# Kernel tuning notes

Measured on AMD Instinct MI355X. Metric: run time of the kernel, lower is better.

The kernel has to match this reference:

```python
import jax, jax.numpy as jnp
import numpy as np

BS, S, WIDTH, MODES = 2, 512, 64, 16
P = S * (S - 1) // 2
IU, JU = np.triu_indices(S, 1)  # upper-triangle (i<j) index constants
COLL_COEF = 0.9  # training=True path


def spectral_conv(x, w):
    # x: (bs, c_in, n), w: (c_in, c_out, modes, 2)
    n = x.shape[-1]
    xf = jnp.fft.rfft(x, axis=2, norm='ortho')  # (bs, c_in, n//2+1) complex
    wm = w[..., 0] + 1j * w[..., 1]
    out_m = jnp.einsum('bix,iox->box', xf[:, :, :MODES], wm)
    pad = jnp.zeros((x.shape[0], w.shape[1], n // 2 + 1 - MODES), dtype=out_m.dtype)
    return jnp.fft.irfft(jnp.concatenate([out_m, pad], axis=2), n=n, axis=2, norm='ortho')


def dsmc(x, a, rvec):
    # x, a: (bs, c, n); rvec: (bs, c, P) unit vectors along c.  dt=1, v = a*dt.
    bs, c, n = x.shape
    v = a
    x_r = jnp.linalg.norm(x[:, :, :, None] - x[:, :, None, :], axis=1)  # (bs, n, n)
    v_r = jnp.linalg.norm(v[:, :, :, None] - v[:, :, None, :], axis=1)
    v_cm = (v[:, :, :, None] + v[:, :, None, :]) * 0.5  # (bs, c, n, n)
    x_cm = (x[:, :, :, None] + x[:, :, None, :]) * 0.5
    u_x = jnp.exp(-x_r)
    v_r_max = jnp.max(v_r, axis=(1, 2), keepdims=True)  # (bs,1,1)
    mask = v_r / v_r_max * u_x
    cm = mask > (1.0 - COLL_COEF)  # collision mask (bs, n, n)
    # antisymmetric projection of v_r upper triangle onto random unit vectors
    proj = v_r[:, IU, JU][:, None, :] * rvec  # (bs, c, P)
    vrl = (jnp.zeros((bs, c, n, n), x.dtype)
           .at[:, :, IU, JU].set(proj)
           .at[:, :, JU, IU].set(-proj))
    delta_v = v_cm + vrl - v[:, :, :, None]
    cmf = cm.astype(x.dtype)
    v_new = v + jnp.sum(delta_v * cmf[:, None], axis=2)  # sum over partners i
    cmf = cmf + jnp.eye(n, dtype=x.dtype)[None]  # add self
    x_new = jnp.sum(x_cm * cmf[:, None], axis=2) / jnp.sum(cmf, axis=2)[:, None, :]
    x_new = x_new + v_new  # x = x + v*dt
    return x_new, v_new


def setup_inputs() -> dict:
    key = jax.random.key(0)
    ks = jax.random.split(key, 12)
    x = jax.random.normal(ks[0], (BS, S, 2), jnp.float32)
    v = jax.random.normal(ks[1], (BS, WIDTH, S), jnp.float32)
    vecs = jax.random.normal(ks[2], (4, BS, WIDTH, P), jnp.float32)
    vecs = vecs / jnp.linalg.norm(vecs, axis=2, keepdims=True)  # unit vectors over chnl
    fc0_w = jax.random.normal(ks[3], (2, WIDTH), jnp.float32) * 0.5
    fc0_b = jax.random.normal(ks[4], (WIDTH,), jnp.float32) * 0.1
    scale = 1.0 / (WIDTH * WIDTH)
    spec_w = jax.random.uniform(ks[5], (4, WIDTH, WIDTH, MODES, 2), jnp.float32) * scale
    conv_w = jax.random.normal(ks[6], (4, WIDTH, WIDTH), jnp.float32) * (WIDTH ** -0.5)
    conv_b = jax.random.normal(ks[7], (4, WIDTH), jnp.float32) * 0.05
    fc1_w = jax.random.normal(ks[8], (WIDTH, 128), jnp.float32) * (WIDTH ** -0.5)
    fc1_b = jnp.zeros((128,), jnp.float32)
    fc2_w = jax.random.normal(ks[9], (128, 1), jnp.float32) * (128 ** -0.5)
    fc2_b = jnp.zeros((1,), jnp.float32)
    return {"x": x, "v": v, "vecs": vecs, "fc0_w": fc0_w, "fc0_b": fc0_b,
            "spec_w": spec_w, "conv_w": conv_w, "conv_b": conv_b,
            "fc1_w": fc1_w, "fc1_b": fc1_b, "fc2_w": fc2_w, "fc2_b": fc2_b}


def reference(x, v, vecs, fc0_w, fc0_b, spec_w, conv_w, conv_b, fc1_w, fc1_b, fc2_w, fc2_b):
    # NOTE: v is overwritten by a*dt inside KINET_DSMC2 in the original; kept for signature fidelity.
    h = x @ fc0_w + fc0_b          # (bs, s, width)
    h = jnp.transpose(h, (0, 2, 1))  # (bs, width, s)
    for i in range(4):
        a = spectral_conv(h, spec_w[i])
        p = jnp.einsum('oi,bin->bon', conv_w[i], h) + conv_b[i][None, :, None]
        h, vv = dsmc(p, a, vecs[i])
        if i < 3:
            h = jax.nn.relu(h)
    h = jnp.transpose(h, (0, 2, 1))  # (bs, s, width)
    h = jax.nn.relu(h @ fc1_w + fc1_b)
    return h @ fc2_w + fc2_b  # (bs, s, 1)
```

## Files before the change

### kernel.cpp

```cpp
#include <hip/hip_runtime.h>
#include <math.h>

#define S 512
#define W 64
#define MODES 16
#define PAIRS 130816
#define INV_SQRT_N 0.04419417382415922f
#define TWO_PI_OVER_N 0.012271846303085130f

__global__ __launch_bounds__(256) void k_fft(const float* __restrict__ h,
                                             const float* __restrict__ x,
                                             const float* __restrict__ fc0w,
                                             const float* __restrict__ fc0b,
                                             float* __restrict__ Xf, int first) {
    int b = blockIdx.x >> 6, ch = blockIdx.x & 63;
    int tid = threadIdx.x;
    float v0, v1;
    if (first) {
        float w0 = fc0w[ch], w1 = fc0w[64 + ch], bb = fc0b[ch];
        const float* xb = x + (size_t)b * S * 2;
        v0 = xb[2 * tid] * w0 + xb[2 * tid + 1] * w1 + bb;
        v1 = xb[2 * (tid + 256)] * w0 + xb[2 * (tid + 256) + 1] * w1 + bb;
    } else {
        const float* hp = h + (b * W + ch) * S;
        v0 = hp[tid]; v1 = hp[tid + 256];
    }
    float re[MODES], im[MODES];
#pragma unroll
    for (int m = 0; m < MODES; ++m) {
        float sn, cs;
        sincosf(TWO_PI_OVER_N * (float)(m * tid), &sn, &cs);
        float a = (m & 1) ? (v0 - v1) : (v0 + v1);
        re[m] = a * cs;
        im[m] = -a * sn;
    }
    __shared__ float part[4][32];
    int lane = tid & 63, wv = tid >> 6;
#pragma unroll
    for (int m = 0; m < MODES; ++m) {
        float r = re[m], ii = im[m];
        for (int off = 32; off; off >>= 1) {
            r += __shfl_down(r, off);
            ii += __shfl_down(ii, off);
        }
        if (lane == 0) { part[wv][2 * m] = r; part[wv][2 * m + 1] = ii; }
    }
    __syncthreads();
    if (tid < 32) {
        float s = part[0][tid] + part[1][tid] + part[2][tid] + part[3][tid];
        Xf[(b * W + ch) * 32 + tid] = s * INV_SQRT_N;
    }
}

__global__ __launch_bounds__(256) void k_mix(const float* __restrict__ Xf,
                                             const float* __restrict__ specw,
                                             float* __restrict__ Y, int l) {
    int b = blockIdx.x >> 6, o = blockIdx.x & 63;
    int tid = threadIdx.x, m = tid & 15, ip = tid >> 4;
    __shared__ float Xs[2048];
    for (int idx = tid; idx < 2048; idx += 256) Xs[idx] = Xf[b * 2048 + idx];
    __syncthreads();
    float ar = 0.f, ai = 0.f;
#pragma unroll
    for (int q = 0; q < 4; ++q) {
        int i = ip * 4 + q;
        const float* wp = specw + (size_t)(((l * W + i) * W + o) * MODES + m) * 2;
        float wr = wp[0], wi = wp[1];
        float xr = Xs[i * 32 + 2 * m], xi = Xs[i * 32 + 2 * m + 1];
        ar += xr * wr - xi * wi;
        ai += xr * wi + xi * wr;
    }
    __shared__ float redr[16][17], redi[16][17];
    redr[ip][m] = ar; redi[ip][m] = ai;
    __syncthreads();
    if (tid < 16) {
        float sr = 0.f, si = 0.f;
        for (int p = 0; p < 16; ++p) { sr += redr[p][tid]; si += redi[p][tid]; }
        Y[(b * W + o) * 32 + 2 * tid] = sr;
        Y[(b * W + o) * 32 + 2 * tid + 1] = si;
    }
}

__global__ __launch_bounds__(256) void k_ac(const float* __restrict__ Y,
                                            const float* __restrict__ h,
                                            const float* __restrict__ x,
                                            const float* __restrict__ fc0w,
                                            const float* __restrict__ fc0b,
                                            const float* __restrict__ convw,
                                            const float* __restrict__ convb,
                                            float* __restrict__ aT,
                                            float* __restrict__ pT,
                                            unsigned* __restrict__ vmax,
                                            int l, int first) {
    int blk = blockIdx.x;
    int b = blk >> 7, t0 = (blk & 127) * 4;
    int tid = threadIdx.x;
    int o = tid & 63, tg = tid >> 6;
    if (blk == 0 && tid < 2) vmax[tid] = 0u;
    __shared__ float hs[64 * 5];
    {
        int r = tid >> 2, t = tid & 3;
        if (first) {
            const float* xb = x + ((size_t)b * S + t0 + t) * 2;
            hs[r * 5 + t] = xb[0] * fc0w[r] + xb[1] * fc0w[64 + r] + fc0b[r];
        } else {
            hs[r * 5 + t] = h[(b * W + r) * S + t0 + t];
        }
    }
    float yr[MODES], yi[MODES];
    const float4* yp = (const float4*)(Y + b * 2048 + o * 32);
#pragma unroll
    for (int q = 0; q < 8; ++q) {
        float4 y4 = yp[q];
        yr[2 * q] = y4.x; yi[2 * q] = y4.y;
        yr[2 * q + 1] = y4.z; yi[2 * q + 1] = y4.w;
    }
    int t = t0 + tg;
    float acc = yr[0];
#pragma unroll
    for (int m = 1; m < MODES; ++m) {
        float sn, cs;
        sincosf(TWO_PI_OVER_N * (float)(m * t), &sn, &cs);
        acc += 2.0f * (yr[m] * cs - yi[m] * sn);
    }
    aT[((size_t)b * S + t) * W + o] = acc * INV_SQRT_N;
    __syncthreads();
    float pacc = convb[l * W + o];
    const float4* wp = (const float4*)(convw + l * 4096 + o * 64);
#pragma unroll
    for (int i4 = 0; i4 < 16; ++i4) {
        float4 w4 = wp[i4];
        pacc = fmaf(w4.x, hs[(4 * i4 + 0) * 5 + tg], pacc);
        pacc = fmaf(w4.y, hs[(4 * i4 + 1) * 5 + tg], pacc);
        pacc = fmaf(w4.z, hs[(4 * i4 + 2) * 5 + tg], pacc);
        pacc = fmaf(w4.w, hs[(4 * i4 + 3) * 5 + tg], pacc);
    }
    pT[((size_t)b * S + t) * W + o] = pacc;
}

__global__ __launch_bounds__(256) void k_pair(const float* __restrict__ pT,
                                              const float* __restrict__ aT,
                                              float* __restrict__ vr,
                                              float* __restrict__ uxm,
                                              unsigned* __restrict__ vmax) {
    int blk = blockIdx.x;
    int b = blk >> 8;
    int rest = blk & 255;
    int i0 = (rest & 15) * 32, j0 = (rest >> 4) * 32;
    int tid = threadIdx.x;
    int tx = tid & 15, ty = tid >> 4;
    __shared__ float Pi[64 * 33], Pj[64 * 33], Vi[64 * 33], Vj[64 * 33];
    for (int idx = tid; idx < 2048; idx += 256) {
        int k = idx >> 6, c = idx & 63;
        Pi[c * 33 + k] = pT[(b * S + i0 + k) * W + c];
        Pj[c * 33 + k] = pT[(b * S + j0 + k) * W + c];
        Vi[c * 33 + k] = aT[(b * S + i0 + k) * W + c];
        Vj[c * 33 + k] = aT[(b * S + j0 + k) * W + c];
    }
    __syncthreads();
    float ax[2][2] = {{0.f, 0.f}, {0.f, 0.f}};
    float av[2][2] = {{0.f, 0.f}, {0.f, 0.f}};
    for (int c = 0; c < W; ++c) {
        float pi0 = Pi[c * 33 + 2 * tx], pi1 = Pi[c * 33 + 2 * tx + 1];
        float pj0 = Pj[c * 33 + 2 * ty], pj1 = Pj[c * 33 + 2 * ty + 1];
        float vi0 = Vi[c * 33 + 2 * tx], vi1 = Vi[c * 33 + 2 * tx + 1];
        float vj0 = Vj[c * 33 + 2 * ty], vj1 = Vj[c * 33 + 2 * ty + 1];
        float d;
        d = pi0 - pj0; ax[0][0] = fmaf(d, d, ax[0][0]);
        d = pi1 - pj0; ax[1][0] = fmaf(d, d, ax[1][0]);
        d = pi0 - pj1; ax[0][1] = fmaf(d, d, ax[0][1]);
        d = pi1 - pj1; ax[1][1] = fmaf(d, d, ax[1][1]);
        d = vi0 - vj0; av[0][0] = fmaf(d, d, av[0][0]);
        d = vi1 - vj0; av[1][0] = fmaf(d, d, av[1][0]);
        d = vi0 - vj1; av[0][1] = fmaf(d, d, av[0][1]);
        d = vi1 - vj1; av[1][1] = fmaf(d, d, av[1][1]);
    }
    float mx = 0.f;
#pragma unroll
    for (int jj = 0; jj < 2; ++jj) {
#pragma unroll
        for (int ii = 0; ii < 2; ++ii) {
            int i = i0 + 2 * tx + ii, j = j0 + 2 * ty + jj;
            float xr = sqrtf(ax[ii][jj]);
            float vv = sqrtf(av[ii][jj]);
            vr[((size_t)b * S + j) * S + i] = vv;
            uxm[((size_t)b * S + j) * S + i] = expf(-xr);
            mx = fmaxf(mx, vv);
        }
    }
    __shared__ float mxs[4];
    for (int off = 32; off; off >>= 1) mx = fmaxf(mx, __shfl_xor(mx, off));
    if ((tid & 63) == 0) mxs[tid >> 6] = mx;
    __syncthreads();
    if (tid == 0) {
        float m = fmaxf(fmaxf(mxs[0], mxs[1]), fmaxf(mxs[2], mxs[3]));
        atomicMax(&vmax[b], __float_as_uint(m));
    }
}

__global__ __launch_bounds__(256) void k_mpf(const float* __restrict__ vr,
                                             const float* __restrict__ uxm,
                                             const unsigned* __restrict__ vmaxu,
                                             const float* __restrict__ aT,
                                             const float* __restrict__ pT,
                                             const float* __restrict__ vecs,
                                             float* __restrict__ h_std,
                                             const float* __restrict__ fc1w,
                                             const float* __restrict__ fc1b,
                                             const float* __restrict__ fc2w,
                                             const float* __restrict__ fc2b,
                                             float* __restrict__ out,
                                             int l, int do_relu, int do_head) {
    int b = blockIdx.x >> 9, q = blockIdx.x & 511;
    int tid = threadIdx.x, lane = tid & 63, wv = tid >> 6;
    __shared__ float wrow[S];
    __shared__ float SV[4][64], SX[4][64], TP[4][64];
    __shared__ float hrow[64];
    __shared__ int cnt4[4];
    const float* vrp = vr + ((size_t)b * S + q) * S;
    const float* uxp = uxm + ((size_t)b * S + q) * S;
    float vmax = __uint_as_float(vmaxu[b]);
    int mycnt = 0;
    for (int i = tid; i < S; i += 256) {
        float v = vrp[i], u = uxp[i];
        bool act = (v / vmax) * u > 0.1f;
        wrow[i] = act ? v : 0.f;
        mycnt += act ? 1 : 0;
    }
    for (int o = 32; o; o >>= 1) mycnt += __shfl_down(mycnt, o);
    if (lane == 0) cnt4[wv] = mycnt;
    __syncthreads();
    float A = (float)(cnt4[0] + cnt4[1] + cnt4[2] + cnt4[3]);
    float svp = 0.f, sxp = 0.f, tp = 0.f;
    const float* aTb = aT + (size_t)b * S * W;
    const float* pTb = pT + (size_t)b * S * W;
    const float* Rb = vecs + (size_t)((l * 2 + b) * W + lane) * PAIRS;
    int triq = q * 511 - ((q * (q - 1)) >> 1);
    for (int k = 0; k < 128; ++k) {
        int p = wv * 128 + k;
        float w = wrow[p];
        if (w != 0.f) {
            svp += aTb[p * W + lane];
            sxp += pTb[p * W + lane];
            int idx; float sgn;
            if (p < q) { idx = p * 511 - ((p * (p - 1)) >> 1) + (q - p - 1); sgn = 1.f; }
            else       { idx = triq + (p - q - 1); sgn = -1.f; }
            tp = fmaf(sgn * w, Rb[idx], tp);
        }
    }
    SV[wv][lane] = svp; SX[wv][lane] = sxp; TP[wv][lane] = tp;
    __syncthreads();
    if (wv == 0) {
        float sv = SV[0][lane] + SV[1][lane] + SV[2][lane] + SV[3][lane];
        float sx = SX[0][lane] + SX[1][lane] + SX[2][lane] + SX[3][lane];
        float T  = TP[0][lane] + TP[1][lane] + TP[2][lane] + TP[3][lane];
        float vj = aTb[q * W + lane], xj = pTb[q * W + lane];
        float vnew = vj + 0.5f * (A * vj - sv) + T;
        float accx = 0.5f * (A * xj + sx);
        float xnew = (xj + accx) / (A + 1.0f) + vnew;
        if (do_relu) xnew = fmaxf(xnew, 0.0f);
        if (!do_head) h_std[((size_t)b * W + lane) * S + q] = xnew;
        else hrow[lane] = xnew;
    }
    if (do_head) {
        __syncthreads();
        if (wv == 0) {
            float a0 = fc1b[lane], a1 = fc1b[lane + 64];
            for (int cc = 0; cc < W; ++cc) {
                float hv = hrow[cc];
                a0 = fmaf(hv, fc1w[cc * 128 + lane], a0);
                a1 = fmaf(hv, fc1w[cc * 128 + lane + 64], a1);
            }
            a0 = fmaxf(a0, 0.f); a1 = fmaxf(a1, 0.f);
            float p = a0 * fc2w[lane] + a1 * fc2w[lane + 64];
            for (int off = 32; off; off >>= 1) p += __shfl_down(p, off);
            if (lane == 0) out[b * S + q] = p + fc2b[0];
        }
    }
}

extern "C" void kernel_launch(void* const* d_in, const int* in_sizes, int n_in,
                              void* d_out, int out_size, void* d_ws, size_t ws_size,
                              hipStream_t stream) {
    const float* x = (const float*)d_in[0];
    const float* vecs = (const float*)d_in[2];
    const float* fc0w = (const float*)d_in[3];
    const float* fc0b = (const float*)d_in[4];
    const float* specw = (const float*)d_in[5];
    const float* convw = (const float*)d_in[6];
    const float* convb = (const float*)d_in[7];
    const float* fc1w = (const float*)d_in[8];
    const float* fc1b = (const float*)d_in[9];
    const float* fc2w = (const float*)d_in[10];
    const float* fc2b = (const float*)d_in[11];
    float* out = (float*)d_out;

    char* ws = (char*)d_ws;
    unsigned* vmax = (unsigned*)ws;
    float* h_std = (float*)(ws + 256);
    float* aT = h_std + 65536;
    float* pT = aT + 65536;
    float* Xf = pT + 65536;
    float* Yb = Xf + 4096;
    float* vrbuf = Yb + 4096;
    float* uxbuf = vrbuf + 524288;

    for (int l = 0; l < 4; ++l) {
        int first = (l == 0) ? 1 : 0;
        k_fft<<<128, 256, 0, stream>>>(h_std, x, fc0w, fc0b, Xf, first);
        k_mix<<<128, 256, 0, stream>>>(Xf, specw, Yb, l);
        k_ac<<<256, 256, 0, stream>>>(Yb, h_std, x, fc0w, fc0b, convw, convb,
                                      aT, pT, vmax, l, first);
        k_pair<<<512, 256, 0, stream>>>(pT, aT, vrbuf, uxbuf, vmax);
        k_mpf<<<1024, 256, 0, stream>>>(vrbuf, uxbuf, vmax, aT, pT, vecs,
                                        h_std, fc1w, fc1b, fc2w, fc2b, out,
                                        l, (l < 3) ? 1 : 0, (l == 3) ? 1 : 0);
    }
}
```

Measured before the change: 655.9 us.

## Fuse spectral mode mixing into inverse-DFT/conv kernel with transposed weights

Removes the separate k_mix launch by folding the complex mode-mixing into the inverse-DFT/pointwise-conv kernel, which now handles 16 timesteps per block instead of 4. A one-time prep kernel transposes the spectral weights for coalesced loads. Twiddles are built in shared memory and advanced by angle-addition recurrence instead of a sincos per mode per step, and k_pair smem padding changes to 34 so it can use float2 loads. The cost is that k_acm runs only 64 blocks (low occupancy) and each block recomputes the mixing redundantly over all 64 input channels, plus one extra kernel launch.

```diff
diff --git a/kernel.cpp b/kernel.cpp
--- a/kernel.cpp
+++ b/kernel.cpp
@@ -7,6 +7,18 @@
 #define PAIRS 130816
 #define INV_SQRT_N 0.04419417382415922f
 #define TWO_PI_OVER_N 0.012271846303085130f
+
+__global__ __launch_bounds__(256) void k_prep(const float* __restrict__ specw,
+                                              float* __restrict__ wmT) {
+    int bi = blockIdx.x;
+    int tid = threadIdx.x, o = tid & 63, tg = tid >> 6;
+#pragma unroll
+    for (int k = 0; k < 4; ++k) {
+        int m = tg * 4 + k;
+        float2 wv = *(const float2*)(specw + (((size_t)bi * 64 + o) * 16 + m) * 2);
+        *(float2*)(wmT + (((size_t)bi * 16 + m) * 64 + o) * 2) = wv;
+    }
+}
 
 __global__ __launch_bounds__(256) void k_fft(const float* __restrict__ h,
                                              const float* __restrict__ x,
@@ -52,90 +64,124 @@
     }
 }
 
-__global__ __launch_bounds__(256) void k_mix(const float* __restrict__ Xf,
-                                             const float* __restrict__ specw,
-                                             float* __restrict__ Y, int l) {
-    int b = blockIdx.x >> 6, o = blockIdx.x & 63;
-    int tid = threadIdx.x, m = tid & 15, ip = tid >> 4;
-    __shared__ float Xs[2048];
-    for (int idx = tid; idx < 2048; idx += 256) Xs[idx] = Xf[b * 2048 + idx];
-    __syncthreads();
-    float ar = 0.f, ai = 0.f;
-#pragma unroll
-    for (int q = 0; q < 4; ++q) {
-        int i = ip * 4 + q;
-        const float* wp = specw + (size_t)(((l * W + i) * W + o) * MODES + m) * 2;
-        float wr = wp[0], wi = wp[1];
-        float xr = Xs[i * 32 + 2 * m], xi = Xs[i * 32 + 2 * m + 1];
-        ar += xr * wr - xi * wi;
-        ai += xr * wi + xi * wr;
-    }
-    __shared__ float redr[16][17], redi[16][17];
-    redr[ip][m] = ar; redi[ip][m] = ai;
-    __syncthreads();
-    if (tid < 16) {
-        float sr = 0.f, si = 0.f;
-        for (int p = 0; p < 16; ++p) { sr += redr[p][tid]; si += redi[p][tid]; }
-        Y[(b * W + o) * 32 + 2 * tid] = sr;
-        Y[(b * W + o) * 32 + 2 * tid + 1] = si;
-    }
-}
-
-__global__ __launch_bounds__(256) void k_ac(const float* __restrict__ Y,
-                                            const float* __restrict__ h,
-                                            const float* __restrict__ x,
-                                            const float* __restrict__ fc0w,
-                                            const float* __restrict__ fc0b,
-                                            const float* __restrict__ convw,
-                                            const float* __restrict__ convb,
-                                            float* __restrict__ aT,
-                                            float* __restrict__ pT,
-                                            unsigned* __restrict__ vmax,
-                                            int l, int first) {
+__global__ __launch_bounds__(256) void k_acm(const float* __restrict__ Xf,
+                                             const float* __restrict__ wmT,
+                                             const float* __restrict__ h,
+                                             const float* __restrict__ x,
+                                             const float* __restrict__ fc0w,
+                                             const float* __restrict__ fc0b,
+                                             const float* __restrict__ convw,
+                                             const float* __restrict__ convb,
+                                             float* __restrict__ aT,
+                                             float* __restrict__ pT,
+                                             unsigned* __restrict__ vmax,
+                                             int l, int first) {
     int blk = blockIdx.x;
-    int b = blk >> 7, t0 = (blk & 127) * 4;
+    int b = blk >> 5, t0 = (blk & 31) * 16;
     int tid = threadIdx.x;
     int o = tid & 63, tg = tid >> 6;
     if (blk == 0 && tid < 2) vmax[tid] = 0u;
-    __shared__ float hs[64 * 5];
+    __shared__ __align__(16) float Xs[2048];
+    __shared__ __align__(16) float Ys[64 * 34];
+    __shared__ __align__(16) float hs[64][17];
+    __shared__ __align__(16) float trig[256];
+    for (int idx = tid; idx < 2048; idx += 256) Xs[idx] = Xf[b * 2048 + idx];
     {
-        int r = tid >> 2, t = tid & 3;
+        int r = tid >> 2, tq = (tid & 3) * 4;
         if (first) {
-            const float* xb = x + ((size_t)b * S + t0 + t) * 2;
-            hs[r * 5 + t] = xb[0] * fc0w[r] + xb[1] * fc0w[64 + r] + fc0b[r];
+#pragma unroll
+            for (int k = 0; k < 4; ++k) {
+                int t = t0 + tq + k;
+                const float* xb = x + ((size_t)b * S + t) * 2;
+                hs[r][tq + k] = xb[0] * fc0w[r] + xb[1] * fc0w[64 + r] + fc0b[r];
+            }
         } else {
-            hs[r * 5 + t] = h[(b * W + r) * S + t0 + t];
-        }
-    }
+            const float4 h4 = *(const float4*)(h + (b * W + r) * S + t0 + tq);
+            hs[r][tq] = h4.x; hs[r][tq + 1] = h4.y;
+            hs[r][tq + 2] = h4.z; hs[r][tq + 3] = h4.w;
+        }
+    }
+    if (tid < 60) {
+        int m = 1 + (tid % 15), tgr = tid / 15;
+        float sn, cs;
+        sincosf(TWO_PI_OVER_N * (float)(m * (t0 + tgr)), &sn, &cs);
+        trig[(tgr * 15 + (m - 1)) * 2] = cs;
+        trig[(tgr * 15 + (m - 1)) * 2 + 1] = sn;
+    } else if (tid >= 64 && tid < 79) {
+        int m = tid - 63;
+        float sn, cs;
+        sincosf(TWO_PI_OVER_N * (float)(4 * m), &sn, &cs);
+        trig[120 + (m - 1) * 2] = cs;
+        trig[120 + (m - 1) * 2 + 1] = sn;
+    }
+    __syncthreads();
+    {
+        float ar[4] = {0.f, 0.f, 0.f, 0.f}, ai[4] = {0.f, 0.f, 0.f, 0.f};
+        for (int i = 0; i < 64; ++i) {
+            const float2* wp = (const float2*)wmT + (((size_t)(l * 64 + i) * 16 + tg * 4) * 64 + o);
+#pragma unroll
+            for (int mm = 0; mm < 4; ++mm) {
+                float2 wv = wp[(size_t)mm * 64];
+                float2 xv = *(const float2*)&Xs[i * 32 + (tg * 4 + mm) * 2];
+                ar[mm] += xv.x * wv.x - xv.y * wv.y;
+                ai[mm] += xv.x * wv.y + xv.y * wv.x;
+            }
+        }
+#pragma unroll
+        for (int mm = 0; mm < 4; ++mm) {
+            float2 yv; yv.x = ar[mm]; yv.y = ai[mm];
+            *(float2*)&Ys[o * 34 + 2 * (tg * 4 + mm)] = yv;
+        }
+    }
+    __syncthreads();
     float yr[MODES], yi[MODES];
-    const float4* yp = (const float4*)(Y + b * 2048 + o * 32);
-#pragma unroll
-    for (int q = 0; q < 8; ++q) {
-        float4 y4 = yp[q];
-        yr[2 * q] = y4.x; yi[2 * q] = y4.y;
-        yr[2 * q + 1] = y4.z; yi[2 * q + 1] = y4.w;
-    }
-    int t = t0 + tg;
-    float acc = yr[0];
+#pragma unroll
+    for (int m = 0; m < MODES; ++m) {
+        float2 yv = *(const float2*)&Ys[o * 34 + 2 * m];
+        yr[m] = yv.x; yi[m] = yv.y;
+    }
+    float cc[MODES], ss[MODES];
 #pragma unroll
     for (int m = 1; m < MODES; ++m) {
-        float sn, cs;
-        sincosf(TWO_PI_OVER_N * (float)(m * t), &sn, &cs);
-        acc += 2.0f * (yr[m] * cs - yi[m] * sn);
-    }
-    aT[((size_t)b * S + t) * W + o] = acc * INV_SQRT_N;
-    __syncthreads();
-    float pacc = convb[l * W + o];
-    const float4* wp = (const float4*)(convw + l * 4096 + o * 64);
-#pragma unroll
-    for (int i4 = 0; i4 < 16; ++i4) {
-        float4 w4 = wp[i4];
-        pacc = fmaf(w4.x, hs[(4 * i4 + 0) * 5 + tg], pacc);
-        pacc = fmaf(w4.y, hs[(4 * i4 + 1) * 5 + tg], pacc);
-        pacc = fmaf(w4.z, hs[(4 * i4 + 2) * 5 + tg], pacc);
-        pacc = fmaf(w4.w, hs[(4 * i4 + 3) * 5 + tg], pacc);
-    }
-    pT[((size_t)b * S + t) * W + o] = pacc;
+        cc[m] = trig[(tg * 15 + m - 1) * 2];
+        ss[m] = trig[(tg * 15 + m - 1) * 2 + 1];
+    }
+    float a4[4];
+#pragma unroll
+    for (int k = 0; k < 4; ++k) {
+        float acc = yr[0];
+#pragma unroll
+        for (int m = 1; m < MODES; ++m) {
+            acc += 2.0f * (yr[m] * cc[m] - yi[m] * ss[m]);
+            float cd = trig[120 + (m - 1) * 2], sd = trig[120 + (m - 1) * 2 + 1];
+            float nc = cc[m] * cd - ss[m] * sd;
+            float ns = ss[m] * cd + cc[m] * sd;
+            cc[m] = nc; ss[m] = ns;
+        }
+        a4[k] = acc * INV_SQRT_N;
+    }
+#pragma unroll
+    for (int k = 0; k < 4; ++k)
+        aT[((size_t)b * S + t0 + tg + 4 * k) * W + o] = a4[k];
+    float4 wreg[16];
+    const float4* wp4 = (const float4*)(convw + l * 4096 + o * 64);
+#pragma unroll
+    for (int q = 0; q < 16; ++q) wreg[q] = wp4[q];
+    float bias = convb[l * W + o];
+#pragma unroll
+    for (int k = 0; k < 4; ++k) {
+        int tl = tg + 4 * k;
+        float pacc = bias;
+#pragma unroll
+        for (int q = 0; q < 16; ++q) {
+            float4 w4 = wreg[q];
+            pacc = fmaf(w4.x, hs[4 * q + 0][tl], pacc);
+            pacc = fmaf(w4.y, hs[4 * q + 1][tl], pacc);
+            pacc = fmaf(w4.z, hs[4 * q + 2][tl], pacc);
+            pacc = fmaf(w4.w, hs[4 * q + 3][tl], pacc);
+        }
+        pT[((size_t)b * S + t0 + tl) * W + o] = pacc;
+    }
 }
 
 __global__ __launch_bounds__(256) void k_pair(const float* __restrict__ pT,
@@ -149,31 +195,34 @@
     int i0 = (rest & 15) * 32, j0 = (rest >> 4) * 32;
     int tid = threadIdx.x;
     int tx = tid & 15, ty = tid >> 4;
-    __shared__ float Pi[64 * 33], Pj[64 * 33], Vi[64 * 33], Vj[64 * 33];
+    __shared__ __align__(16) float Pi[64 * 34];
+    __shared__ __align__(16) float Pj[64 * 34];
+    __shared__ __align__(16) float Vi[64 * 34];
+    __shared__ __align__(16) float Vj[64 * 34];
     for (int idx = tid; idx < 2048; idx += 256) {
         int k = idx >> 6, c = idx & 63;
-        Pi[c * 33 + k] = pT[(b * S + i0 + k) * W + c];
-        Pj[c * 33 + k] = pT[(b * S + j0 + k) * W + c];
-        Vi[c * 33 + k] = aT[(b * S + i0 + k) * W + c];
-        Vj[c * 33 + k] = aT[(b * S + j0 + k) * W + c];
+        Pi[c * 34 + k] = pT[(b * S + i0 + k) * W + c];
+        Pj[c * 34 + k] = pT[(b * S + j0 + k) * W + c];
+        Vi[c * 34 + k] = aT[(b * S + i0 + k) * W + c];
+        Vj[c * 34 + k] = aT[(b * S + j0 + k) * W + c];
     }
     __syncthreads();
     float ax[2][2] = {{0.f, 0.f}, {0.f, 0.f}};
     float av[2][2] = {{0.f, 0.f}, {0.f, 0.f}};
     for (int c = 0; c < W; ++c) {
-        float pi0 = Pi[c * 33 + 2 * tx], pi1 = Pi[c * 33 + 2 * tx + 1];
-        float pj0 = Pj[c * 33 + 2 * ty], pj1 = Pj[c * 33 + 2 * ty + 1];
-        float vi0 = Vi[c * 33 + 2 * tx], vi1 = Vi[c * 33 + 2 * tx + 1];
-        float vj0 = Vj[c * 33 + 2 * ty], vj1 = Vj[c * 33 + 2 * ty + 1];
+        float2 pi = *(const float2*)&Pi[c * 34 + 2 * tx];
+        float2 pj = *(const float2*)&Pj[c * 34 + 2 * ty];
+        float2 vi = *(const float2*)&Vi[c * 34 + 2 * tx];
+        float2 vj = *(const float2*)&Vj[c * 34 + 2 * ty];
         float d;
-        d = pi0 - pj0; ax[0][0] = fmaf(d, d, ax[0][0]);
-        d = pi1 - pj0; ax[1][0] = fmaf(d, d, ax[1][0]);
-        d = pi0 - pj1; ax[0][1] = fmaf(d, d, ax[0][1]);
-        d = pi1 - pj1; ax[1][1] = fmaf(d, d, ax[1][1]);
-        d = vi0 - vj0; av[0][0] = fmaf(d, d, av[0][0]);
-        d = vi1 - vj0; av[1][0] = fmaf(d, d, av[1][0]);
-        d = vi0 - vj1; av[0][1] = fmaf(d, d, av[0][1]);
-        d = vi1 - vj1; av[1][1] = fmaf(d, d, av[1][1]);
+        d = pi.x - pj.x; ax[0][0] = fmaf(d, d, ax[0][0]);
+        d = pi.y - pj.x; ax[1][0] = fmaf(d, d, ax[1][0]);
+        d = pi.x - pj.y; ax[0][1] = fmaf(d, d, ax[0][1]);
+        d = pi.y - pj.y; ax[1][1] = fmaf(d, d, ax[1][1]);
+        d = vi.x - vj.x; av[0][0] = fmaf(d, d, av[0][0]);
+        d = vi.y - vj.x; av[1][0] = fmaf(d, d, av[1][0]);
+        d = vi.x - vj.y; av[0][1] = fmaf(d, d, av[0][1]);
+        d = vi.y - vj.y; av[1][1] = fmaf(d, d, av[1][1]);
     }
     float mx = 0.f;
 #pragma unroll
@@ -301,16 +350,16 @@
     float* aT = h_std + 65536;
     float* pT = aT + 65536;
     float* Xf = pT + 65536;
-    float* Yb = Xf + 4096;
-    float* vrbuf = Yb + 4096;
+    float* wmT = Xf + 4096;
+    float* vrbuf = wmT + 524288;
     float* uxbuf = vrbuf + 524288;
 
+    k_prep<<<256, 256, 0, stream>>>(specw, wmT);
     for (int l = 0; l < 4; ++l) {
         int first = (l == 0) ? 1 : 0;
         k_fft<<<128, 256, 0, stream>>>(h_std, x, fc0w, fc0b, Xf, first);
-        k_mix<<<128, 256, 0, stream>>>(Xf, specw, Yb, l);
-        k_ac<<<256, 256, 0, stream>>>(Yb, h_std, x, fc0w, fc0b, convw, convb,
-                                      aT, pT, vmax, l, first);
+        k_acm<<<64, 256, 0, stream>>>(Xf, wmT, h_std, x, fc0w, fc0b,
+                                      convw, convb, aT, pT, vmax, l, first);
         k_pair<<<512, 256, 0, stream>>>(pT, aT, vrbuf, uxbuf, vmax);
         k_mpf<<<1024, 256, 0, stream>>>(vrbuf, uxbuf, vmax, aT, pT, vecs,
                                         h_std, fc1w, fc1b, fc2w, fc2b, out,
```

Result: slower. 701.1 us (+6.9%).
